# Optimization experiments

Hardware: AMD Instinct MI355X
Metric: run time of the kernel (lower is better)

The kernel has to match this reference:

```python
import jax, jax.numpy as jnp
import numpy as np

M, N, K = 8, 4096, 16  # samples, simplices (Laplacian dim), n_filters


def setup_inputs() -> dict:
    key = jax.random.key(0)
    kx, kl, kw = jax.random.split(key, 3)
    x = jax.random.normal(kx, (M, N, N), dtype=jnp.float32)   # stacked x_list
    L = jax.random.normal(kl, (N, N), dtype=jnp.float32)      # Laplacian
    W = 0.01 * jax.random.normal(kw, (K, N), dtype=jnp.float32)  # filter weights
    return {"x": x, "L": L, "W": W}


def reference(x, L, W):
    # Original math per sample x_b [n,n]:
    #   Lx[i,j]   = (L @ x_b[i])[j] = sum_m L[j,m] x_b[i,m]
    #   weighted  = diag(w_k) @ Lx          -> row i scaled by w_k[i]
    #   filt_out  = act(sum_j weighted[i,j]) = act(w_k[i] * sum_j Lx[i,j])
    # sum_j Lx[i,j] = x_b[i] . colsum(L), so the dense [n,n] diag matmul
    # collapses to a matvec + broadcasted scale (same math, fused form).
    col = jnp.sum(L, axis=0)                       # [n]
    s = jnp.einsum('bim,m->bi', x, col)            # [M, n]
    # sum over filters of tanh(w_k * s)
    out = jnp.sum(jnp.tanh(W[None, :, :] * s[:, None, :]), axis=1)  # [M, n]
    return out
```

## Files before the change

kernel.cpp:

```cpp
#include <hip/hip_runtime.h>

#define NN 4096
#define MM 8
#define KK 16

typedef float v4f __attribute__((ext_vector_type(4)));

__global__ void __launch_bounds__(256) colsum_kernel(const float* __restrict__ L,
                                                     float* __restrict__ col) {
    const int m4 = blockIdx.x * 256 + threadIdx.x;
    const int r0 = blockIdx.y * 16;
    const v4f* __restrict__ L4 = reinterpret_cast<const v4f*>(L);
    v4f acc = {0.f, 0.f, 0.f, 0.f};
#pragma unroll
    for (int j = 0; j < 16; ++j) {
        const v4f v = __builtin_nontemporal_load(&L4[(size_t)(r0 + j) * (NN / 4) + m4]);
        acc += v;
    }
    atomicAdd(&col[m4 * 4 + 0], acc.x);
    atomicAdd(&col[m4 * 4 + 1], acc.y);
    atomicAdd(&col[m4 * 4 + 2], acc.z);
    atomicAdd(&col[m4 * 4 + 3], acc.w);
}

__global__ void __launch_bounds__(256) conv_kernel(const float* __restrict__ x,
                                                   const float* __restrict__ col,
                                                   const float* __restrict__ W,
                                                   float* __restrict__ out) {
    const int wave = threadIdx.x >> 6;
    const int lane = threadIdx.x & 63;
    const int row  = blockIdx.x * 4 + wave;
    const int i    = row & (NN - 1);

    const v4f* __restrict__ xr = reinterpret_cast<const v4f*>(x) + (size_t)row * (NN / 4);
    const v4f* __restrict__ cv = reinterpret_cast<const v4f*>(col);

    float acc = 0.f;
#pragma unroll
    for (int it = 0; it < NN / 4 / 64; ++it) {
        const v4f a = __builtin_nontemporal_load(&xr[it * 64 + lane]);
        const v4f c = cv[it * 64 + lane];
        const v4f p = a * c;
        acc += p.x + p.y + p.z + p.w;
    }

#pragma unroll
    for (int off = 32; off >= 1; off >>= 1)
        acc += __shfl_xor(acc, off, 64);

    float r = 0.f;
    if (lane < KK) r = tanhf(W[lane * NN + i] * acc);
#pragma unroll
    for (int off = 8; off >= 1; off >>= 1)
        r += __shfl_down(r, off, 64);

    if (lane == 0) out[row] = r;
}

extern "C" void kernel_launch(void* const* d_in, const int* in_sizes, int n_in,
                              void* d_out, int out_size, void* d_ws, size_t ws_size,
                              hipStream_t stream) {
    const float* x = (const float*)d_in[0];
    const float* L = (const float*)d_in[1];
    const float* W = (const float*)d_in[2];
    float* out = (float*)d_out;
    float* col = (float*)d_ws;

    (void)hipMemsetAsync(col, 0, NN * sizeof(float), stream);

    colsum_kernel<<<dim3(4, 256), 256, 0, stream>>>(L, col);
    conv_kernel<<<(MM * NN) / 4, 256, 0, stream>>>(x, col, W, out);
}
```

Baseline: 123.7 us.

## Replace atomic colsum with two-stage reduction and pre-transpose W for coalesced reads

The column sum of L becomes a deterministic two-stage reduction that writes per-block partials to workspace, removing the memset and the float atomics. The second stage also transposes W into an [i][k] layout so each wave reads its 16 filter weights contiguously instead of with a 4096-element stride. Nontemporal loads on x and L are dropped in favor of ordinary loads. This adds an extra kernel launch and a workspace round trip for the partials and the transposed W.

```diff
diff --git a/kernel.cpp b/kernel.cpp
--- a/kernel.cpp
+++ b/kernel.cpp
@@ -6,26 +6,48 @@
 
 typedef float v4f __attribute__((ext_vector_type(4)));
 
-__global__ void __launch_bounds__(256) colsum_kernel(const float* __restrict__ L,
-                                                     float* __restrict__ col) {
+#define WS_COL     0
+#define WS_PARTIAL 4096
+#define WS_WT      (4096 + 64 * 4096)
+
+__global__ void __launch_bounds__(256) colsum_stage1(const float* __restrict__ L,
+                                                     float* __restrict__ ws) {
     const int m4 = blockIdx.x * 256 + threadIdx.x;
-    const int r0 = blockIdx.y * 16;
+    const int r0 = blockIdx.y * 64;
     const v4f* __restrict__ L4 = reinterpret_cast<const v4f*>(L);
     v4f acc = {0.f, 0.f, 0.f, 0.f};
-#pragma unroll
-    for (int j = 0; j < 16; ++j) {
-        const v4f v = __builtin_nontemporal_load(&L4[(size_t)(r0 + j) * (NN / 4) + m4]);
-        acc += v;
+#pragma unroll 8
+    for (int j = 0; j < 64; ++j) {
+        acc += L4[(size_t)(r0 + j) * (NN / 4) + m4];
     }
-    atomicAdd(&col[m4 * 4 + 0], acc.x);
-    atomicAdd(&col[m4 * 4 + 1], acc.y);
-    atomicAdd(&col[m4 * 4 + 2], acc.z);
-    atomicAdd(&col[m4 * 4 + 3], acc.w);
+    reinterpret_cast<v4f*>(ws + WS_PARTIAL)[blockIdx.y * (NN / 4) + m4] = acc;
+}
+
+__global__ void __launch_bounds__(256) colsum_stage2(const float* __restrict__ W,
+                                                     float* __restrict__ ws) {
+    const int b = blockIdx.x;
+    const int t = threadIdx.x;
+    if (b < 4) {
+        const int slot = b * 256 + t;
+        const v4f* __restrict__ p4 = reinterpret_cast<const v4f*>(ws + WS_PARTIAL);
+        v4f acc = {0.f, 0.f, 0.f, 0.f};
+#pragma unroll 8
+        for (int j = 0; j < 64; ++j) {
+            acc += p4[j * (NN / 4) + slot];
+        }
+        reinterpret_cast<v4f*>(ws + WS_COL)[slot] = acc;
+    } else {
+        float* __restrict__ Wt = ws + WS_WT;
+        for (int o = (b - 4) * 256 + t; o < NN * KK; o += 12 * 256) {
+            const int i = o >> 4;
+            const int k = o & 15;
+            Wt[o] = W[k * NN + i];
+        }
+    }
 }
 
 __global__ void __launch_bounds__(256) conv_kernel(const float* __restrict__ x,
-                                                   const float* __restrict__ col,
-                                                   const float* __restrict__ W,
+                                                   const float* __restrict__ ws,
                                                    float* __restrict__ out) {
     const int wave = threadIdx.x >> 6;
     const int lane = threadIdx.x & 63;
@@ -33,12 +55,12 @@
     const int i    = row & (NN - 1);
 
     const v4f* __restrict__ xr = reinterpret_cast<const v4f*>(x) + (size_t)row * (NN / 4);
-    const v4f* __restrict__ cv = reinterpret_cast<const v4f*>(col);
+    const v4f* __restrict__ cv = reinterpret_cast<const v4f*>(ws + WS_COL);
 
     float acc = 0.f;
 #pragma unroll
     for (int it = 0; it < NN / 4 / 64; ++it) {
-        const v4f a = __builtin_nontemporal_load(&xr[it * 64 + lane]);
+        const v4f a = xr[it * 64 + lane];
         const v4f c = cv[it * 64 + lane];
         const v4f p = a * c;
         acc += p.x + p.y + p.z + p.w;
@@ -49,7 +71,7 @@
         acc += __shfl_xor(acc, off, 64);
 
     float r = 0.f;
-    if (lane < KK) r = tanhf(W[lane * NN + i] * acc);
+    if (lane < KK) r = tanhf((ws + WS_WT)[i * KK + lane] * acc);
 #pragma unroll
     for (int off = 8; off >= 1; off >>= 1)
         r += __shfl_down(r, off, 64);
@@ -64,10 +86,9 @@
     const float* L = (const float*)d_in[1];
     const float* W = (const float*)d_in[2];
     float* out = (float*)d_out;
-    float* col = (float*)d_ws;
+    float* ws  = (float*)d_ws;
 
-    (void)hipMemsetAsync(col, 0, NN * sizeof(float), stream);
-
-    colsum_kernel<<<dim3(4, 256), 256, 0, stream>>>(L, col);
-    conv_kernel<<<(MM * NN) / 4, 256, 0, stream>>>(x, col, W, out);
+    colsum_stage1<<<dim3(4, 64), 256, 0, stream>>>(L, ws);
+    colsum_stage2<<<16, 256, 0, stream>>>(W, ws);
+    conv_kernel<<<(MM * NN) / 4, 256, 0, stream>>>(x, ws, out);
 }
```

After: 111.6 us. -9.7%, faster.
